# Performance work log

Measured on AMD Instinct MI355X. Metric: run time of the kernel, lower is better.

Reference implementation:

```python
import math
import jax, jax.numpy as jnp
import numpy as np

B, CI, CO, K, WD, H = 8, 512, 512, 3, 512, 64


def setup_inputs() -> dict:
    key = jax.random.key(0)
    ks = jax.random.split(key, 8)
    x = jax.random.normal(ks[0], (B, CI, H, H), jnp.float32)
    style = jax.random.normal(ks[1], (B, WD), jnp.float32)
    noise = jax.random.normal(ks[2], (B, CO, H, H), jnp.float32)
    # learned params
    weight = jax.random.normal(ks[3], (1, CO, CI, K, K), jnp.float32)      # ModulatedConv2d.weight
    mod_weight = jax.random.normal(ks[4], (CI, WD), jnp.float32)            # EqualLinear.weight
    mod_bias = jnp.ones((CI,), jnp.float32)                                  # bias_init=1
    noise_weight = 0.1 * jnp.ones((1,), jnp.float32)                         # NoiseInjection.weight (nonzero for signal)
    act_bias = 0.01 * jax.random.normal(ks[5], (CO,), jnp.float32)           # FusedLeakyReLU.bias
    return {"x": x, "style": style, "noise": noise, "weight": weight,
            "mod_weight": mod_weight, "mod_bias": mod_bias,
            "noise_weight": noise_weight, "act_bias": act_bias}


def reference(x, style, noise, weight, mod_weight, mod_bias, noise_weight, act_bias):
    # EqualLinear modulation: scale = 1/sqrt(w_space_dim), lr_mul = 1
    eq_scale = 1.0 / math.sqrt(WD)
    s = style @ (mod_weight * eq_scale).T + mod_bias            # [B, CI]
    # modulate + demodulate per-sample weights
    conv_scale = 1.0 / math.sqrt(CI * K * K)                     # 1/sqrt(fan_in)
    w = conv_scale * weight * s[:, None, :, None, None]          # [B, CO, CI, K, K]
    demod = jax.lax.rsqrt(jnp.sum(w * w, axis=(2, 3, 4)) + 1e-8)  # [B, CO]
    w = w * demod[:, :, None, None, None]
    pad = K // 2

    def conv1(xi, wi):  # per-sample conv (equivalent to groups=batch trick)
        return jax.lax.conv_general_dilated(
            xi[None], wi, window_strides=(1, 1),
            padding=[(pad, pad), (pad, pad)],
            dimension_numbers=("NCHW", "OIHW", "NCHW"))[0]

    out = jax.vmap(conv1)(x, w)                                  # [B, CO, H, H]
    # noise injection (noise provided -> no normalization branch)
    out = out + noise_weight[0] * noise
    # fused leaky relu: leaky_relu(out + bias) * sqrt(2)
    out = jax.nn.leaky_relu(out + act_bias[None, :, None, None], 0.2) * math.sqrt(2.0)
    return out
```

## Files before the change

kernel.cpp:

```cpp
#include <hip/hip_runtime.h>
#include <hip/hip_bf16.h>

typedef unsigned short u16;
typedef short bf16x8 __attribute__((ext_vector_type(8)));
typedef float f32x4 __attribute__((ext_vector_type(4)));

#define EQ_SCALE   0.04419417382415922f
#define CONV_SCALE 0.014731391274719738f

#define WS_S   0
#define WS_ESC (16*1024)
#define WS_WSQ (32*1024)
#define WS_WT  (32*1024 + 1024*1024)
#define WS_XS  (WS_WT + 9*512*512*2)

__device__ __forceinline__ void gld16(void* l, const void* g) {
  __builtin_amdgcn_global_load_lds((const __attribute__((address_space(1))) void*)g,
                                   (__attribute__((address_space(3))) void*)l,
                                   16, 0, 0);
}

__device__ __forceinline__ u16 f2b_rne(float f) {
  union { float f; unsigned int i; } c; c.f = f;
  unsigned int r = (c.i + 0x7FFFu + ((c.i >> 16) & 1u)) >> 16;
  return (u16)r;
}

__global__ void k_style(const float* __restrict__ style, const float* __restrict__ mw,
                        const float* __restrict__ mb, float* __restrict__ s) {
  int idx = blockIdx.x * 256 + threadIdx.x;
  int b = idx >> 9, i = idx & 511;
  const float* sr = style + (b << 9);
  const float* wr = mw + (i << 9);
  float acc = 0.f;
  for (int j = 0; j < 512; ++j) acc += sr[j] * wr[j];
  s[idx] = acc * EQ_SCALE + mb[i];
}

__global__ void k_wsq(const float* __restrict__ w, float* __restrict__ wsq) {
  int idx = blockIdx.x * 256 + threadIdx.x;
  const float* p = w + idx * 9;
  float a = 0.f;
  for (int t = 0; t < 9; ++t) { float v = p[t]; a += v * v; }
  wsq[idx] = a;
}

__global__ void k_esc(const float* __restrict__ wsq, const float* __restrict__ s,
                      float* __restrict__ esc) {
  int idx = blockIdx.x * 256 + threadIdx.x;
  int b = idx >> 9, o = idx & 511;
  const float* wr = wsq + (o << 9);
  const float* sr = s + (b << 9);
  float a = 0.f;
  for (int i = 0; i < 512; ++i) { float sv = sr[i]; a += wr[i] * sv * sv; }
  esc[idx] = CONV_SCALE * rsqrtf(CONV_SCALE * CONV_SCALE * a + 1e-8f);
}

__global__ void k_wt(const float* __restrict__ w, u16* __restrict__ wt) {
  int idx = blockIdx.x * 256 + threadIdx.x;
  const float* p = w + idx * 9;
  for (int t = 0; t < 9; ++t) wt[t * 262144 + idx] = f2b_rne(p[t]);
}

__global__ void k_xs(const float* __restrict__ x, const float* __restrict__ s,
                     u16* __restrict__ xs) {
  __shared__ u16 tile[64 * 66];
  int by = blockIdx.x;
  int i0 = blockIdx.y << 6;
  int b = by >> 6, y = by & 63;
  int t = threadIdx.x, w = t >> 6, lane = t & 63;
  for (int k = 0; k < 16; ++k) {
    int il = w + (k << 2);
    int i = i0 + il;
    float v = x[((((b << 9) + i) << 6) | y) << 6 | lane] * s[(b << 9) + i];
    tile[lane * 66 + il] = f2b_rne(v);
  }
  __syncthreads();
  for (int k = 0; k < 16; ++k) {
    int xc = w + (k << 2);
    xs[((((b << 6) | y) << 6 | xc) << 9) + i0 + lane] = tile[xc * 66 + lane];
  }
}

__global__ void __launch_bounds__(512, 2) k_conv(
    const u16* __restrict__ wt, const u16* __restrict__ xs,
    const float* __restrict__ esc, const float* __restrict__ noise,
    const float* __restrict__ nwp, const float* __restrict__ abias,
    float* __restrict__ out) {
  __shared__ __align__(16) u16 ldsA[2][128 * 64];
  __shared__ __align__(16) u16 ldsB[2][384 * 64];

  const int t = threadIdx.x;
  const int w = t >> 6, lane = t & 63;
  const int wm = w >> 2, wn = w & 3;
  const int quad = lane >> 4, l15 = lane & 15;
  const int o0 = blockIdx.x << 7;
  const int nt = blockIdx.y;
  const int b = nt >> 4, y0 = (nt & 15) << 2;

  int bgOff[6];
#pragma unroll
  for (int j = 0; j < 6; ++j) {
    int c = j * 512 + t;
    int pos = c >> 3, swz = c & 7;
    int ci16 = swz ^ (pos & 7);
    int tr = pos >> 6, col = pos & 63;
    int yy = y0 - 1 + tr; yy = yy < 0 ? 0 : (yy > 63 ? 63 : yy);
    bgOff[j] = ((((b << 6) + yy) << 6) + col) * 512 + ci16 * 8;
  }
  int agOff[2];
#pragma unroll
  for (int j = 0; j < 2; ++j) {
    int c = j * 512 + t;
    int ol = c >> 3, swz = c & 7;
    int ci16 = swz ^ (ol & 7);
    agOff[j] = (o0 + ol) * 512 + ci16 * 8;
  }

  f32x4 acc[16];
#pragma unroll
  for (int i = 0; i < 16; ++i) acc[i] = (f32x4)0.f;

  int aBase[4], aXor[4];
#pragma unroll
  for (int mf = 0; mf < 4; ++mf) {
    int ol = wm * 64 + mf * 16 + l15;
    aBase[mf] = ol * 8;
    aXor[mf] = ol & 7;
  }

#pragma unroll
  for (int j = 0; j < 6; ++j)
    gld16(&ldsB[0][(j * 512 + w * 64) * 8], xs + bgOff[j]);
#pragma unroll
  for (int j = 0; j < 2; ++j)
    gld16(&ldsA[0][(j * 512 + w * 64) * 8], wt + agOff[j]);

#pragma unroll 1
  for (int cib = 0; cib < 8; ++cib) {
    const u16* bR = ldsB[cib & 1];
#pragma unroll
    for (int khw = 0; khw < 9; ++khw) {
      const int par = (cib + khw) & 1;
      __syncthreads();

      if (cib < 7 || khw < 8) {
        const int nkhw = (khw == 8) ? 0 : khw + 1;
        const int ncib = (khw == 8) ? cib + 1 : cib;
        u16* aW = (u16*)ldsA[par ^ 1];
#pragma unroll
        for (int j = 0; j < 2; ++j)
          gld16(aW + (j * 512 + w * 64) * 8,
                wt + agOff[j] + nkhw * 262144 + ncib * 64);
      }
      if (khw == 6 && cib < 7) {
        u16* bW = (u16*)ldsB[(cib & 1) ^ 1];
#pragma unroll
        for (int j = 0; j < 6; ++j)
          gld16(bW + (j * 512 + w * 64) * 8, xs + bgOff[j] + (cib + 1) * 64);
      }

      const u16* aR = ldsA[par];
      const int kh = khw / 3, kw = khw % 3;
      const int row_in = y0 + wn + kh - 1;
      if (row_in >= 0 && row_in < 64) {
        const int tr = wn + kh;
        int bBase[4], bXor[4];
        bool bz[4];
#pragma unroll
        for (int nf = 0; nf < 4; ++nf) {
          int colo = nf * 16 + l15;
          int ci = colo + kw - 1;
          bz[nf] = (ci < 0) | (ci > 63);
          ci &= 63;
          int pos = tr * 64 + ci;
          bBase[nf] = pos * 8;
          bXor[nf] = pos & 7;
        }
#pragma unroll
        for (int ks = 0; ks < 2; ++ks) {
          const int kci = ks * 4 + quad;
          bf16x8 af[4], bf[4];
#pragma unroll
          for (int mf = 0; mf < 4; ++mf)
            af[mf] = *(const bf16x8*)(aR + (aBase[mf] + (kci ^ aXor[mf])) * 8);
#pragma unroll
          for (int nf = 0; nf < 4; ++nf) {
            bf16x8 v = *(const bf16x8*)(bR + (bBase[nf] + (kci ^ bXor[nf])) * 8);
            bf16x8 z = {0, 0, 0, 0, 0, 0, 0, 0};
            bf[nf] = bz[nf] ? z : v;
          }
          __builtin_amdgcn_s_setprio(1);
#pragma unroll
          for (int mf = 0; mf < 4; ++mf)
#pragma unroll
            for (int nf = 0; nf < 4; ++nf)
              acc[mf * 4 + nf] = __builtin_amdgcn_mfma_f32_16x16x32_bf16(
                  af[mf], bf[nf], acc[mf * 4 + nf], 0, 0, 0);
          __builtin_amdgcn_s_setprio(0);
        }
      }
    }
  }

  const float nwv = nwp[0];
  const int y = y0 + wn;
#pragma unroll
  for (int mf = 0; mf < 4; ++mf) {
#pragma unroll
    for (int r = 0; r < 4; ++r) {
      int o = o0 + wm * 64 + mf * 16 + quad * 4 + r;
      float es = esc[(b << 9) + o];
      float ab = abias[o];
      int rowbase = ((((b << 9) + o) << 6) | y) << 6;
#pragma unroll
      for (int nf = 0; nf < 4; ++nf) {
        int col = nf * 16 + l15;
        int idx = rowbase | col;
        float v = acc[mf * 4 + nf][r] * es + nwv * noise[idx] + ab;
        v = (v < 0.f ? 0.2f * v : v) * 1.4142135623730951f;
        out[idx] = v;
      }
    }
  }
}

extern "C" void kernel_launch(void* const* d_in, const int* in_sizes, int n_in,
                              void* d_out, int out_size, void* d_ws, size_t ws_size,
                              hipStream_t stream) {
  const float* x      = (const float*)d_in[0];
  const float* style  = (const float*)d_in[1];
  const float* noise  = (const float*)d_in[2];
  const float* weight = (const float*)d_in[3];
  const float* mw     = (const float*)d_in[4];
  const float* mb     = (const float*)d_in[5];
  const float* nw     = (const float*)d_in[6];
  const float* ab     = (const float*)d_in[7];
  float* out = (float*)d_out;

  char* ws = (char*)d_ws;
  float* s   = (float*)(ws + WS_S);
  float* esc = (float*)(ws + WS_ESC);
  float* wsq = (float*)(ws + WS_WSQ);
  u16* wt    = (u16*)(ws + WS_WT);
  u16* xs    = (u16*)(ws + WS_XS);

  k_style<<<16, 256, 0, stream>>>(style, mw, mb, s);
  k_wsq<<<1024, 256, 0, stream>>>(weight, wsq);
  k_esc<<<16, 256, 0, stream>>>(wsq, s, esc);
  k_wt<<<1024, 256, 0, stream>>>(weight, wt);
  k_xs<<<dim3(512, 8), 256, 0, stream>>>(x, s, xs);
  k_conv<<<dim3(4, 128), 512, 0, stream>>>(wt, xs, esc, noise, nw, ab, out);
}
```

Before: 395.2 us.

## Load weights directly into registers in MFMA layout, enlarge tile to 256 outputs

Pre-permutes the bf16 weights so each lane can read its MFMA A fragment straight from global memory. This removes the A-tile LDS staging and the per-khw barrier. The output tile per block doubles to 256 channels, with each wave covering 64x128 and 32 accumulators. Block IDs are remapped so blocks sharing an XCD share the same output-channel half. Out-of-range padding rows now read from a zeroed scratch buffer instead of being branched around. This trades LDS traffic and syncs for more register pressure, heavier global/L2 traffic for weights, and half as many blocks.

```diff
diff --git a/kernel.cpp b/kernel.cpp
--- a/kernel.cpp
+++ b/kernel.cpp
@@ -2,6 +2,7 @@
 #include <hip/hip_bf16.h>
 
 typedef unsigned short u16;
+typedef unsigned long long u64;
 typedef short bf16x8 __attribute__((ext_vector_type(8)));
 typedef float f32x4 __attribute__((ext_vector_type(4)));
 
@@ -13,6 +14,7 @@
 #define WS_WSQ (32*1024)
 #define WS_WT  (32*1024 + 1024*1024)
 #define WS_XS  (WS_WT + 9*512*512*2)
+#define WS_Z   (WS_XS + 8*64*64*512*2)
 
 __device__ __forceinline__ void gld16(void* l, const void* g) {
   __builtin_amdgcn_global_load_lds((const __attribute__((address_space(1))) void*)g,
@@ -56,10 +58,20 @@
   esc[idx] = CONV_SCALE * rsqrtf(CONV_SCALE * CONV_SCALE * a + 1e-8f);
 }
 
-__global__ void k_wt(const float* __restrict__ w, u16* __restrict__ wt) {
-  int idx = blockIdx.x * 256 + threadIdx.x;
+__global__ void k_zero(u64* __restrict__ z) {
+  z[blockIdx.x * 256 + threadIdx.x] = 0ull;
+}
+
+__global__ void k_wt(const float* __restrict__ w, u16* __restrict__ wt2) {
+  int idx = blockIdx.x * 256 + threadIdx.x;
+  int o = idx >> 9, ci = idx & 511;
   const float* p = w + idx * 9;
-  for (int t = 0; t < 9; ++t) wt[t * 262144 + idx] = f2b_rne(p[t]);
+  int og = o >> 4;
+  int lane = (o & 15) | (((ci >> 3) & 3) << 4);
+  int cib = ci >> 6, ks = (ci >> 5) & 1, j = ci & 7;
+  int base = cib * 32768 + og * 1024 + ks * 512 + lane * 8 + j;
+  for (int khw = 0; khw < 9; ++khw)
+    wt2[khw * 262144 + base] = f2b_rne(p[khw]);
 }
 
 __global__ void k_xs(const float* __restrict__ x, const float* __restrict__ s,
@@ -83,128 +95,109 @@
 }
 
 __global__ void __launch_bounds__(512, 2) k_conv(
-    const u16* __restrict__ wt, const u16* __restrict__ xs,
+    const u16* __restrict__ wt2, const u16* __restrict__ xs,
+    const u16* __restrict__ zbuf,
     const float* __restrict__ esc, const float* __restrict__ noise,
     const float* __restrict__ nwp, const float* __restrict__ abias,
     float* __restrict__ out) {
-  __shared__ __align__(16) u16 ldsA[2][128 * 64];
   __shared__ __align__(16) u16 ldsB[2][384 * 64];
 
   const int t = threadIdx.x;
   const int w = t >> 6, lane = t & 63;
-  const int wm = w >> 2, wn = w & 3;
+  const int wm = w >> 1, wn = w & 1;
   const int quad = lane >> 4, l15 = lane & 15;
-  const int o0 = blockIdx.x << 7;
-  const int nt = blockIdx.y;
+  const int wn2 = wn << 1;
+
+  const int flat = blockIdx.y * 2 + blockIdx.x;
+  const int xcd = flat & 7, sgrp = flat >> 3;
+  const int o0 = (xcd >> 2) << 8;
+  const int nt = sgrp * 4 + (xcd & 3);
   const int b = nt >> 4, y0 = (nt & 15) << 2;
 
-  int bgOff[6];
+  const u16* bgp[6];
 #pragma unroll
   for (int j = 0; j < 6; ++j) {
     int c = j * 512 + t;
     int pos = c >> 3, swz = c & 7;
     int ci16 = swz ^ (pos & 7);
-    int tr = pos >> 6, col = pos & 63;
-    int yy = y0 - 1 + tr; yy = yy < 0 ? 0 : (yy > 63 ? 63 : yy);
-    bgOff[j] = ((((b << 6) + yy) << 6) + col) * 512 + ci16 * 8;
-  }
-  int agOff[2];
-#pragma unroll
-  for (int j = 0; j < 2; ++j) {
-    int c = j * 512 + t;
-    int ol = c >> 3, swz = c & 7;
-    int ci16 = swz ^ (ol & 7);
-    agOff[j] = (o0 + ol) * 512 + ci16 * 8;
-  }
-
-  f32x4 acc[16];
-#pragma unroll
-  for (int i = 0; i < 16; ++i) acc[i] = (f32x4)0.f;
-
-  int aBase[4], aXor[4];
-#pragma unroll
-  for (int mf = 0; mf < 4; ++mf) {
-    int ol = wm * 64 + mf * 16 + l15;
-    aBase[mf] = ol * 8;
-    aXor[mf] = ol & 7;
-  }
+    int col = pos & 63;
+    int yy = y0 - 1 + j;
+    if ((unsigned)yy < 64u)
+      bgp[j] = xs + ((((b << 6) + yy) << 6) + col) * 512 + ci16 * 8;
+    else
+      bgp[j] = zbuf + col * 512 + ci16 * 8;
+  }
+
+  const int aoff = o0 * 64 + wm * 4096 + lane * 8;
+
+  f32x4 acc[32];
+#pragma unroll
+  for (int i = 0; i < 32; ++i) acc[i] = (f32x4)0.f;
 
 #pragma unroll
   for (int j = 0; j < 6; ++j)
-    gld16(&ldsB[0][(j * 512 + w * 64) * 8], xs + bgOff[j]);
-#pragma unroll
-  for (int j = 0; j < 2; ++j)
-    gld16(&ldsA[0][(j * 512 + w * 64) * 8], wt + agOff[j]);
+    gld16(&ldsB[0][(j * 512 + w * 64) * 8], bgp[j]);
 
 #pragma unroll 1
   for (int cib = 0; cib < 8; ++cib) {
-    const u16* bR = ldsB[cib & 1];
+    __syncthreads();
+    const u16* bR = &ldsB[cib & 1][0];
 #pragma unroll
     for (int khw = 0; khw < 9; ++khw) {
-      const int par = (cib + khw) & 1;
-      __syncthreads();
-
-      if (cib < 7 || khw < 8) {
-        const int nkhw = (khw == 8) ? 0 : khw + 1;
-        const int ncib = (khw == 8) ? cib + 1 : cib;
-        u16* aW = (u16*)ldsA[par ^ 1];
-#pragma unroll
-        for (int j = 0; j < 2; ++j)
-          gld16(aW + (j * 512 + w * 64) * 8,
-                wt + agOff[j] + nkhw * 262144 + ncib * 64);
-      }
-      if (khw == 6 && cib < 7) {
-        u16* bW = (u16*)ldsB[(cib & 1) ^ 1];
+      const int kh = khw / 3, kw = khw % 3;
+      const u16* wp = wt2 + (khw * 8 + cib) * 32768 + aoff;
+
+      bf16x8 af[2][4];
+#pragma unroll
+      for (int ks = 0; ks < 2; ++ks)
+#pragma unroll
+        for (int mf = 0; mf < 4; ++mf)
+          af[ks][mf] = *(const bf16x8*)(wp + mf * 1024 + ks * 512);
+
+      if (khw == 7 && cib < 7) {
+        u16* bW = &ldsB[(cib & 1) ^ 1][0];
 #pragma unroll
         for (int j = 0; j < 6; ++j)
-          gld16(bW + (j * 512 + w * 64) * 8, xs + bgOff[j] + (cib + 1) * 64);
-      }
-
-      const u16* aR = ldsA[par];
-      const int kh = khw / 3, kw = khw % 3;
-      const int row_in = y0 + wn + kh - 1;
-      if (row_in >= 0 && row_in < 64) {
-        const int tr = wn + kh;
-        int bBase[4], bXor[4];
-        bool bz[4];
-#pragma unroll
-        for (int nf = 0; nf < 4; ++nf) {
-          int colo = nf * 16 + l15;
-          int ci = colo + kw - 1;
-          bz[nf] = (ci < 0) | (ci > 63);
-          ci &= 63;
-          int pos = tr * 64 + ci;
-          bBase[nf] = pos * 8;
-          bXor[nf] = pos & 7;
+          gld16(bW + (j * 512 + w * 64) * 8, bgp[j] + (cib + 1) * 64);
+      }
+
+      int bBase[8], bXor[8];
+      unsigned cmask[8];
+#pragma unroll
+      for (int nf = 0; nf < 8; ++nf) {
+        const int r = nf >> 2, cg = nf & 3;
+        const int tr = wn2 + r + kh;
+        int ci = cg * 16 + l15 + kw - 1;
+        cmask[nf] = ((kw == 0 && cg == 0) || (kw == 2 && cg == 3))
+                        ? (unsigned)((unsigned)ci > 63u) : 0u;
+        ci &= 63;
+        int pos = tr * 64 + ci;
+        bBase[nf] = pos * 8;
+        bXor[nf] = pos & 7;
+      }
+#pragma unroll
+      for (int ks = 0; ks < 2; ++ks) {
+        const int kci = ks * 4 + quad;
+        bf16x8 bv[8];
+#pragma unroll
+        for (int nf = 0; nf < 8; ++nf) {
+          bf16x8 v = *(const bf16x8*)(bR + (bBase[nf] + (kci ^ bXor[nf])) * 8);
+          bf16x8 z = {0, 0, 0, 0, 0, 0, 0, 0};
+          bv[nf] = cmask[nf] ? z : v;
         }
-#pragma unroll
-        for (int ks = 0; ks < 2; ++ks) {
-          const int kci = ks * 4 + quad;
-          bf16x8 af[4], bf[4];
-#pragma unroll
-          for (int mf = 0; mf < 4; ++mf)
-            af[mf] = *(const bf16x8*)(aR + (aBase[mf] + (kci ^ aXor[mf])) * 8);
-#pragma unroll
-          for (int nf = 0; nf < 4; ++nf) {
-            bf16x8 v = *(const bf16x8*)(bR + (bBase[nf] + (kci ^ bXor[nf])) * 8);
-            bf16x8 z = {0, 0, 0, 0, 0, 0, 0, 0};
-            bf[nf] = bz[nf] ? z : v;
-          }
-          __builtin_amdgcn_s_setprio(1);
-#pragma unroll
-          for (int mf = 0; mf < 4; ++mf)
-#pragma unroll
-            for (int nf = 0; nf < 4; ++nf)
-              acc[mf * 4 + nf] = __builtin_amdgcn_mfma_f32_16x16x32_bf16(
-                  af[mf], bf[nf], acc[mf * 4 + nf], 0, 0, 0);
-          __builtin_amdgcn_s_setprio(0);
-        }
+        __builtin_amdgcn_s_setprio(1);
+#pragma unroll
+        for (int mf = 0; mf < 4; ++mf)
+#pragma unroll
+          for (int nf = 0; nf < 8; ++nf)
+            acc[mf * 8 + nf] = __builtin_amdgcn_mfma_f32_16x16x32_bf16(
+                af[ks][mf], bv[nf], acc[mf * 8 + nf], 0, 0, 0);
+        __builtin_amdgcn_s_setprio(0);
       }
     }
   }
 
   const float nwv = nwp[0];
-  const int y = y0 + wn;
 #pragma unroll
   for (int mf = 0; mf < 4; ++mf) {
 #pragma unroll
@@ -212,12 +205,12 @@
       int o = o0 + wm * 64 + mf * 16 + quad * 4 + r;
       float es = esc[(b << 9) + o];
       float ab = abias[o];
-      int rowbase = ((((b << 9) + o) << 6) | y) << 6;
-#pragma unroll
-      for (int nf = 0; nf < 4; ++nf) {
-        int col = nf * 16 + l15;
-        int idx = rowbase | col;
-        float v = acc[mf * 4 + nf][r] * es + nwv * noise[idx] + ab;
+#pragma unroll
+      for (int nf = 0; nf < 8; ++nf) {
+        int y = y0 + wn2 + (nf >> 2);
+        int col = (nf & 3) * 16 + l15;
+        int idx = ((((((b << 9) + o) << 6) | y)) << 6) | col;
+        float v = acc[mf * 8 + nf][r] * es + nwv * noise[idx] + ab;
         v = (v < 0.f ? 0.2f * v : v) * 1.4142135623730951f;
         out[idx] = v;
       }
@@ -242,13 +235,15 @@
   float* s   = (float*)(ws + WS_S);
   float* esc = (float*)(ws + WS_ESC);
   float* wsq = (float*)(ws + WS_WSQ);
-  u16* wt    = (u16*)(ws + WS_WT);
+  u16* wt2   = (u16*)(ws + WS_WT);
   u16* xs    = (u16*)(ws + WS_XS);
-
+  u16* zbuf  = (u16*)(ws + WS_Z);
+
+  k_zero<<<32, 256, 0, stream>>>((u64*)zbuf);
   k_style<<<16, 256, 0, stream>>>(style, mw, mb, s);
   k_wsq<<<1024, 256, 0, stream>>>(weight, wsq);
   k_esc<<<16, 256, 0, stream>>>(wsq, s, esc);
-  k_wt<<<1024, 256, 0, stream>>>(weight, wt);
+  k_wt<<<1024, 256, 0, stream>>>(weight, wt2);
   k_xs<<<dim3(512, 8), 256, 0, stream>>>(x, s, xs);
-  k_conv<<<dim3(4, 128), 512, 0, stream>>>(wt, xs, esc, noise, nw, ab, out);
-}
+  k_conv<<<dim3(2, 128), 512, 0, stream>>>(wt2, xs, zbuf, esc, noise, nw, ab, out);
+}
```

After: 488.6 us. +23.6%, slower.
